# Optimization experiments

Hardware: AMD Instinct MI355X
Metric: run time of the kernel (lower is better)

Reference implementation:

```python
import jax, jax.numpy as jnp
import numpy as np

NUM_HEADS = 16

def _rope_tables(seq_len, head_dim):
    # inv_freq over even indices; freqs = outer(t, inv_freq) -> [S, head_dim//2]
    inv_freq = 1.0 / (10000.0 ** (jnp.arange(0, head_dim, 2, dtype=jnp.float32) / head_dim))
    t = jnp.arange(seq_len, dtype=jnp.float32)
    freqs = t[:, None] * inv_freq[None, :]
    return jnp.cos(freqs), jnp.sin(freqs)  # each [S, head_dim//2]

def _apply_rope(x, cos, sin):
    # x: [B,H,S,hd]; cos/sin: [S, hd//2] broadcast to [1,1,S,hd//2]
    hd = x.shape[-1]
    x1, x2 = x[..., : hd // 2], x[..., hd // 2 :]
    c = cos[None, None]
    s = sin[None, None]
    return jnp.concatenate([x1 * c - x2 * s, x2 * c + x1 * s], axis=-1)

def setup_inputs() -> dict:
    key = jax.random.key(0)
    k1, k2, k3 = jax.random.split(key, 3)
    B, S, D = 2, 2048, 1024
    x = jax.random.normal(k1, (B, S, D), dtype=jnp.float32)
    w_qkv = jax.random.normal(k2, (3 * D, D), dtype=jnp.float32) * (2.0 / D) ** 0.5
    w_out = jax.random.normal(k3, (D, D), dtype=jnp.float32) * (2.0 / D) ** 0.5
    b_out = jnp.zeros((D,), dtype=jnp.float32)
    return {"x": x, "w_qkv": w_qkv, "w_out": w_out, "b_out": b_out}

def reference(x, w_qkv, w_out, b_out):
    B, S, D = x.shape
    H = NUM_HEADS
    hd = D // H
    scale = hd ** -0.5
    qkv = jnp.einsum("bsd,ed->bse", x, w_qkv)  # [B,S,3D]
    qkv = qkv.reshape(B, S, 3, H, hd).transpose(2, 0, 3, 1, 4)  # [3,B,H,S,hd]
    q, k, v = qkv[0], qkv[1], qkv[2]
    cos, sin = _rope_tables(S, hd)
    q = _apply_rope(q, cos, sin)
    k = _apply_rope(k, cos, sin)
    scores = jnp.einsum("bhqd,bhkd->bhqk", q, k) * scale  # [B,H,S,S]
    attn = jax.nn.softmax(scores, axis=-1)
    out = jnp.einsum("bhqk,bhkd->bhqd", attn, v)  # [B,H,S,hd]
    out = out.transpose(0, 2, 1, 3).reshape(B, S, D)
    return jnp.einsum("bsd,ed->bse", out, w_out) + b_out
```

## Files before the change

kernel.cpp:

```cpp
#include <hip/hip_runtime.h>
#include <hip/hip_bf16.h>
#include <math.h>

typedef __bf16 bf16;
typedef __attribute__((ext_vector_type(8))) __bf16 bf16x8;
typedef __attribute__((ext_vector_type(4))) __bf16 bf16x4;
typedef __attribute__((ext_vector_type(4))) float f32x4;
typedef __attribute__((ext_vector_type(16))) float f32x16;

#define MFMA16(a, b, c) __builtin_amdgcn_mfma_f32_16x16x32_bf16((a), (b), (c), 0, 0, 0)
#define MFMA32(a, b, c) __builtin_amdgcn_mfma_f32_32x32x16_bf16((a), (b), (c), 0, 0, 0)

__device__ __forceinline__ float fexp2(float x) { return __builtin_amdgcn_exp2f(x); }

__device__ __forceinline__ int swz(int row, int col) {
  return row * 64 + ((((col) >> 3) ^ (row & 7)) << 3) + (col & 7);
}

__device__ __forceinline__ void gl_lds16(const bf16* g, bf16* l) {
  __builtin_amdgcn_global_load_lds(
      (const __attribute__((address_space(1))) void*)g,
      (__attribute__((address_space(3))) void*)l, 16, 0, 0);
}

__global__ __launch_bounds__(256) void cvt_all(const float* __restrict__ x,
                                               const float* __restrict__ wq,
                                               const float* __restrict__ wo,
                                               bf16* __restrict__ xb,
                                               bf16* __restrict__ wqb,
                                               bf16* __restrict__ wob) {
  int i = blockIdx.x * 256 + threadIdx.x;
  const float* src;
  bf16* dst;
  int off;
  if (i < 1048576)       { src = x;  dst = xb;  off = i; }
  else if (i < 1835008)  { src = wq; dst = wqb; off = i - 1048576; }
  else                   { src = wo; dst = wob; off = i - 1835008; }
  float4 v = ((const float4*)src)[off];
  bf16x4 o = {(bf16)v.x, (bf16)v.y, (bf16)v.z, (bf16)v.w};
  ((bf16x4*)dst)[off] = o;
}

__global__ __launch_bounds__(256) void gemm_bt(const bf16* __restrict__ A,
                                               const bf16* __restrict__ Bm,
                                               float* __restrict__ Cf,
                                               const float* __restrict__ bias,
                                               int M, int N, int K) {
  __shared__ __align__(16) bf16 As[128 * 64];
  __shared__ __align__(16) bf16 Bs[128 * 64];
  const int t = threadIdx.x;
  const int w = t >> 6, l = t & 63;
  const int wr = w >> 1, wc = w & 1;
  const int lr = l & 15, lh = l >> 4;
  const int bm = blockIdx.x * 128, bn = blockIdx.y * 128;
  const int srow = l >> 3;
  const int schunk = (l & 7) ^ srow;

  f32x4 acc[4][4] = {};

  for (int k0 = 0; k0 < K; k0 += 64) {
    __syncthreads();
#pragma unroll
    for (int jj = 0; jj < 4; ++jj) {
      const int j = w + jj * 4;
      const int r = j * 8 + srow;
      gl_lds16(A + (size_t)(bm + r) * K + k0 + schunk * 8, As + j * 512);
      gl_lds16(Bm + (size_t)(bn + r) * K + k0 + schunk * 8, Bs + j * 512);
    }
    __syncthreads();
#pragma unroll
    for (int kk = 0; kk < 2; ++kk) {
      bf16x8 af[4], bfr[4];
#pragma unroll
      for (int mt = 0; mt < 4; ++mt)
        af[mt] = *(const bf16x8*)(As + swz(wr * 64 + mt * 16 + lr, kk * 32 + lh * 8));
#pragma unroll
      for (int nt = 0; nt < 4; ++nt)
        bfr[nt] = *(const bf16x8*)(Bs + swz(wc * 64 + nt * 16 + lr, kk * 32 + lh * 8));
#pragma unroll
      for (int mt = 0; mt < 4; ++mt)
#pragma unroll
        for (int nt = 0; nt < 4; ++nt)
          acc[mt][nt] = MFMA16(af[mt], bfr[nt], acc[mt][nt]);
    }
  }

#pragma unroll
  for (int mt = 0; mt < 4; ++mt)
#pragma unroll
    for (int nt = 0; nt < 4; ++nt)
#pragma unroll
      for (int r = 0; r < 4; ++r) {
        int m = bm + wr * 64 + mt * 16 + lh * 4 + r;
        int n = bn + wc * 64 + nt * 16 + lr;
        Cf[(size_t)m * N + n] = acc[mt][nt][r] + bias[n];
      }
}

__global__ __launch_bounds__(256) void gemm_qkv_rope(const bf16* __restrict__ A,
                                                     const bf16* __restrict__ Bm,
                                                     bf16* __restrict__ Qd,
                                                     bf16* __restrict__ Kd,
                                                     bf16* __restrict__ Vtg) {
  const int K = 1024;
  __shared__ __align__(16) bf16 As[128 * 64];
  __shared__ __align__(16) bf16 Bs[128 * 64];
  const int t = threadIdx.x;
  const int w = t >> 6, l = t & 63;
  const int wr = w >> 1, wc = w & 1;
  const int lr = l & 15, lh = l >> 4;
  const int bm = blockIdx.x * 128, bn = blockIdx.y * 128;
  const int srow = l >> 3;
  const int schunk = (l & 7) ^ srow;

  f32x4 acc[4][4] = {};

  for (int k0 = 0; k0 < K; k0 += 64) {
    __syncthreads();
#pragma unroll
    for (int jj = 0; jj < 4; ++jj) {
      const int j = w + jj * 4;
      const int r = j * 8 + srow;
      gl_lds16(A + (size_t)(bm + r) * K + k0 + schunk * 8, As + j * 512);
      gl_lds16(Bm + (size_t)(bn + r) * K + k0 + schunk * 8, Bs + j * 512);
    }
    __syncthreads();
#pragma unroll
    for (int kk = 0; kk < 2; ++kk) {
      bf16x8 af[4], bfr[4];
#pragma unroll
      for (int mt = 0; mt < 4; ++mt)
        af[mt] = *(const bf16x8*)(As + swz(wr * 64 + mt * 16 + lr, kk * 32 + lh * 8));
#pragma unroll
      for (int nt = 0; nt < 4; ++nt)
        bfr[nt] = *(const bf16x8*)(Bs + swz(wc * 64 + nt * 16 + lr, kk * 32 + lh * 8));
#pragma unroll
      for (int mt = 0; mt < 4; ++mt)
#pragma unroll
        for (int nt = 0; nt < 4; ++nt)
          acc[mt][nt] = MFMA16(af[mt], bfr[nt], acc[mt][nt]);
    }
  }

  const int b = bm >> 11;
  const int sbase = (bm & 2047) + wr * 64 + lh * 4;
  const int sec = bn >> 10;
  const int h = ((bn & 1023) + wc * 64) >> 6;
  const int bh = b * 16 + h;

  if (sec < 2) {
    bf16* dst = (sec == 0 ? Qd : Kd) + (size_t)bh * 2048 * 64;
    const float QSs = sec == 0 ? 0.18033688011112042f : 1.0f;
#pragma unroll
    for (int nt = 0; nt < 2; ++nt) {
      const int j = nt * 16 + lr;
      const float ifr = fexp2((float)j * -0.4152410118609203f) *
                        0.15915494309189535f;
#pragma unroll
      for (int mt = 0; mt < 4; ++mt) {
#pragma unroll
        for (int r = 0; r < 4; ++r) {
          const int s = sbase + mt * 16 + r;
          float rev = (float)s * ifr;
          rev -= floorf(rev);
          float c  = __builtin_amdgcn_cosf(rev);
          float sn = __builtin_amdgcn_sinf(rev);
          float x1 = acc[mt][nt][r], x2 = acc[mt][nt + 2][r];
          dst[(size_t)s * 64 + j]      = (bf16)((x1 * c - x2 * sn) * QSs);
          dst[(size_t)s * 64 + j + 32] = (bf16)((x2 * c + x1 * sn) * QSs);
        }
      }
    }
  } else {
    bf16* dst = Vtg + (size_t)bh * 131072;
#pragma unroll
    for (int nt = 0; nt < 4; ++nt) {
      const int d = nt * 16 + lr;
#pragma unroll
      for (int mt = 0; mt < 4; ++mt) {
        const int g = sbase + mt * 16;
        const int gp = (g & ~12) | ((g & 4) << 1) | ((g & 8) >> 1);
        bf16x4 v4 = {(bf16)acc[mt][nt][0], (bf16)acc[mt][nt][1],
                     (bf16)acc[mt][nt][2], (bf16)acc[mt][nt][3]};
        *(bf16x4*)(dst + (size_t)d * 2048 + gp) = v4;
      }
    }
  }
}

__global__ __launch_bounds__(256) void attn_fwd(const bf16* __restrict__ Qg,
                                                const bf16* __restrict__ Kg,
                                                const bf16* __restrict__ Vtg,
                                                bf16* __restrict__ Og) {
  __shared__ __align__(16) bf16 Ks[32 * 128];
  __shared__ __align__(16) bf16 Vt[32 * 128];
  const int bh = blockIdx.x, qt = blockIdx.y;
  const int t = threadIdx.x, wv = t >> 6, l = t & 63;
  const int lq = l & 31, hi = l >> 5;
  const bf16* Qb  = Qg  + (size_t)bh * 2048 * 64;
  const bf16* Kb  = Kg  + (size_t)bh * 2048 * 64;
  const bf16* Vtb = Vtg + (size_t)bh * 131072;
  const int q = qt * 128 + wv * 32 + lq;

  bf16x8 qf[4];
#pragma unroll
  for (int s = 0; s < 4; ++s)
    qf[s] = *(const bf16x8*)(Qb + (size_t)q * 64 + s * 16 + hi * 8);

  bf16x8 onesf;
#pragma unroll
  for (int e = 0; e < 8; ++e) onesf[e] = (bf16)1.0f;

  f32x16 o0 = {}, o1 = {};
  f32x16 lacc = {};

  const int r0 = t >> 2, c0 = (t & 3) * 16;
  const int srow = r0 & 31;
  const int L0 = ((r0 >> 5) << 3) + (c0 >> 3);
  const int off0 = srow * 128 + (((L0)     ^ (r0 & 15)) << 3);
  const int off1 = srow * 128 + (((L0 + 1) ^ (r0 & 15)) << 3);

  bf16x8 kreg0 = *(const bf16x8*)(Kb + (size_t)r0 * 64 + c0);
  bf16x8 kreg1 = *(const bf16x8*)(Kb + (size_t)r0 * 64 + c0 + 8);
  bf16x8 vreg0 = *(const bf16x8*)(Vtb + (size_t)r0 * 2048 + c0);
  bf16x8 vreg1 = *(const bf16x8*)(Vtb + (size_t)r0 * 2048 + c0 + 8);

  for (int tt = 0; tt < 32; ++tt) {
    __syncthreads();
    *(bf16x8*)(Ks + off0) = kreg0;
    *(bf16x8*)(Ks + off1) = kreg1;
    *(bf16x8*)(Vt + off0) = vreg0;
    *(bf16x8*)(Vt + off1) = vreg1;
    __syncthreads();

    if (tt + 1 < 32) {
      const int KV2 = (tt + 1) * 64;
      kreg0 = *(const bf16x8*)(Kb + (size_t)(KV2 + r0) * 64 + c0);
      kreg1 = *(const bf16x8*)(Kb + (size_t)(KV2 + r0) * 64 + c0 + 8);
      vreg0 = *(const bf16x8*)(Vtb + (size_t)r0 * 2048 + KV2 + c0);
      vreg1 = *(const bf16x8*)(Vtb + (size_t)r0 * 2048 + KV2 + c0 + 8);
    }

    f32x16 p0 = {}, p1 = {};
    __builtin_amdgcn_s_setprio(1);
#pragma unroll
    for (int s = 0; s < 4; ++s) {
      bf16x8 ka0 = *(const bf16x8*)(Ks + lq * 128 + (((2 * s + hi) ^ (lq & 15)) << 3));
      bf16x8 ka1 = *(const bf16x8*)(Ks + lq * 128 + (((8 + 2 * s + hi) ^ (lq & 15)) << 3));
      p0 = MFMA32(ka0, qf[s], p0);
      p1 = MFMA32(ka1, qf[s], p1);
    }
    __builtin_amdgcn_s_setprio(0);

#pragma unroll
    for (int j = 0; j < 16; ++j) {
      p0[j] = fexp2(p0[j]);
      p1[j] = fexp2(p1[j]);
    }

    __builtin_amdgcn_s_setprio(1);
#pragma unroll
    for (int s = 0; s < 4; ++s) {
      bf16x8 pb;
#pragma unroll
      for (int e = 0; e < 8; ++e) {
        float pv = (s == 0) ? p0[e] : (s == 1) ? p0[8 + e]
                 : (s == 2) ? p1[e] : p1[8 + e];
        pb[e] = (bf16)pv;
      }
      bf16x8 va0 = *(const bf16x8*)(Vt + lq * 128 + (((2 * s + hi) ^ (lq & 15)) << 3));
      bf16x8 va1 = *(const bf16x8*)(Vt + lq * 128 + (((8 + 2 * s + hi) ^ (lq & 15)) << 3));
      o0 = MFMA32(va0, pb, o0);
      o1 = MFMA32(va1, pb, o1);
      lacc = MFMA32(onesf, pb, lacc);
    }
    __builtin_amdgcn_s_setprio(0);
  }

  float inv = 1.0f / lacc[0];
  const int b = bh >> 4, h = bh & 15;
  bf16* orow = Og + (size_t)(b * 2048 + q) * 1024 + h * 64;
#pragma unroll
  for (int dblk = 0; dblk < 2; ++dblk) {
#pragma unroll
    for (int J = 0; J < 4; ++J) {
      float e0 = (dblk ? o1[4 * J] : o0[4 * J]) * inv;
      float e1 = (dblk ? o1[4 * J + 1] : o0[4 * J + 1]) * inv;
      float e2 = (dblk ? o1[4 * J + 2] : o0[4 * J + 2]) * inv;
      float e3 = (dblk ? o1[4 * J + 3] : o0[4 * J + 3]) * inv;
      bf16x4 wv2 = {(bf16)e0, (bf16)e1, (bf16)e2, (bf16)e3};
      *(bf16x4*)(orow + dblk * 32 + 8 * J + 4 * hi) = wv2;
    }
  }
}

extern "C" void kernel_launch(void* const* d_in, const int* in_sizes, int n_in,
                              void* d_out, int out_size, void* d_ws, size_t ws_size,
                              hipStream_t stream) {
  const float* x     = (const float*)d_in[0];
  const float* w_qkv = (const float*)d_in[1];
  const float* w_out = (const float*)d_in[2];
  const float* b_out = (const float*)d_in[3];
  float* out = (float*)d_out;
  char* ws = (char*)d_ws;
  const size_t MB = 1024 * 1024;

  bf16* xb    = (bf16*)(ws);
  bf16* wqkvb = (bf16*)(ws + 8 * MB);
  bf16* woutb = (bf16*)(ws + 14 * MB);
  bf16* Qd    = (bf16*)(ws + 40 * MB);
  bf16* Kd    = (bf16*)(ws + 48 * MB);
  bf16* Vtg   = (bf16*)(ws + 56 * MB);
  bf16* attnb = xb;

  cvt_all<<<8192, 256, 0, stream>>>(x, w_qkv, w_out, xb, wqkvb, woutb);

  gemm_qkv_rope<<<dim3(32, 24), 256, 0, stream>>>(xb, wqkvb, Qd, Kd, Vtg);
  attn_fwd<<<dim3(32, 16), 256, 0, stream>>>(Qd, Kd, Vtg, attnb);
  gemm_bt<<<dim3(32, 8), 256, 0, stream>>>(attnb, woutb, out, b_out,
                                           4096, 1024, 1024);
}
```

Measured before the change: 123.6 us.

## Double attention block to 512 threads, split K and V staging across halves

The attention kernel now runs 8 waves per block, covering 256 queries instead of 128. The grid is halved so each K/V tile loaded into LDS serves twice as many queries. The first 256 threads stage K and the second 256 stage V, which halves the per-thread global loads and register staging. The cost is fewer blocks (256 instead of 512), which may leave some of the 256 CUs underfed or hurt occupancy, and barriers now synchronize more waves.

```diff
diff --git a/kernel.cpp b/kernel.cpp
--- a/kernel.cpp
+++ b/kernel.cpp
@@ -188,7 +188,7 @@
   }
 }
 
-__global__ __launch_bounds__(256) void attn_fwd(const bf16* __restrict__ Qg,
+__global__ __launch_bounds__(512) void attn_fwd(const bf16* __restrict__ Qg,
                                                 const bf16* __restrict__ Kg,
                                                 const bf16* __restrict__ Vtg,
                                                 bf16* __restrict__ Og) {
@@ -200,7 +200,7 @@
   const bf16* Qb  = Qg  + (size_t)bh * 2048 * 64;
   const bf16* Kb  = Kg  + (size_t)bh * 2048 * 64;
   const bf16* Vtb = Vtg + (size_t)bh * 131072;
-  const int q = qt * 128 + wv * 32 + lq;
+  const int q = qt * 256 + wv * 32 + lq;
 
   bf16x8 qf[4];
 #pragma unroll
@@ -214,31 +214,39 @@
   f32x16 o0 = {}, o1 = {};
   f32x16 lacc = {};
 
-  const int r0 = t >> 2, c0 = (t & 3) * 16;
+  const int vhalf = t >> 8;
+  const int ch = t & 255;
+  const int r0 = ch >> 2, c0 = (ch & 3) * 16;
   const int srow = r0 & 31;
   const int L0 = ((r0 >> 5) << 3) + (c0 >> 3);
   const int off0 = srow * 128 + (((L0)     ^ (r0 & 15)) << 3);
   const int off1 = srow * 128 + (((L0 + 1) ^ (r0 & 15)) << 3);
-
-  bf16x8 kreg0 = *(const bf16x8*)(Kb + (size_t)r0 * 64 + c0);
-  bf16x8 kreg1 = *(const bf16x8*)(Kb + (size_t)r0 * 64 + c0 + 8);
-  bf16x8 vreg0 = *(const bf16x8*)(Vtb + (size_t)r0 * 2048 + c0);
-  bf16x8 vreg1 = *(const bf16x8*)(Vtb + (size_t)r0 * 2048 + c0 + 8);
+  bf16* ldst = vhalf ? Vt : Ks;
+
+  bf16x8 sreg0, sreg1;
+  if (vhalf) {
+    sreg0 = *(const bf16x8*)(Vtb + (size_t)r0 * 2048 + c0);
+    sreg1 = *(const bf16x8*)(Vtb + (size_t)r0 * 2048 + c0 + 8);
+  } else {
+    sreg0 = *(const bf16x8*)(Kb + (size_t)r0 * 64 + c0);
+    sreg1 = *(const bf16x8*)(Kb + (size_t)r0 * 64 + c0 + 8);
+  }
 
   for (int tt = 0; tt < 32; ++tt) {
     __syncthreads();
-    *(bf16x8*)(Ks + off0) = kreg0;
-    *(bf16x8*)(Ks + off1) = kreg1;
-    *(bf16x8*)(Vt + off0) = vreg0;
-    *(bf16x8*)(Vt + off1) = vreg1;
+    *(bf16x8*)(ldst + off0) = sreg0;
+    *(bf16x8*)(ldst + off1) = sreg1;
     __syncthreads();
 
     if (tt + 1 < 32) {
       const int KV2 = (tt + 1) * 64;
-      kreg0 = *(const bf16x8*)(Kb + (size_t)(KV2 + r0) * 64 + c0);
-      kreg1 = *(const bf16x8*)(Kb + (size_t)(KV2 + r0) * 64 + c0 + 8);
-      vreg0 = *(const bf16x8*)(Vtb + (size_t)r0 * 2048 + KV2 + c0);
-      vreg1 = *(const bf16x8*)(Vtb + (size_t)r0 * 2048 + KV2 + c0 + 8);
+      if (vhalf) {
+        sreg0 = *(const bf16x8*)(Vtb + (size_t)r0 * 2048 + KV2 + c0);
+        sreg1 = *(const bf16x8*)(Vtb + (size_t)r0 * 2048 + KV2 + c0 + 8);
+      } else {
+        sreg0 = *(const bf16x8*)(Kb + (size_t)(KV2 + r0) * 64 + c0);
+        sreg1 = *(const bf16x8*)(Kb + (size_t)(KV2 + r0) * 64 + c0 + 8);
+      }
     }
 
     f32x16 p0 = {}, p1 = {};
@@ -316,7 +324,7 @@
   cvt_all<<<8192, 256, 0, stream>>>(x, w_qkv, w_out, xb, wqkvb, woutb);
 
   gemm_qkv_rope<<<dim3(32, 24), 256, 0, stream>>>(xb, wqkvb, Qd, Kd, Vtg);
-  attn_fwd<<<dim3(32, 16), 256, 0, stream>>>(Qd, Kd, Vtg, attnb);
+  attn_fwd<<<dim3(32, 8), 512, 0, stream>>>(Qd, Kd, Vtg, attnb);
   gemm_bt<<<dim3(32, 8), 256, 0, stream>>>(attnb, woutb, out, b_out,
                                            4096, 1024, 1024);
 }
```

Measured after the change: 116.9 us. 1.06x faster.
